# Kernel tuning notes

Measured on AMD Instinct MI355X. Metric: run time of the kernel, lower is better.

Reference implementation:

```python
import jax, jax.numpy as jnp
import numpy as np

BOX = 8.0  # side length of the box points are sampled in
N_POINTS = 12288
N_BINS_TARGET = 10


def setup_inputs() -> dict:
    key = jax.random.key(0)
    k1, k2 = jax.random.split(key)
    pc = jax.random.uniform(k1, (N_POINTS, 3), dtype=jnp.float32) * BOX
    target_rdf = jax.random.uniform(k2, (N_BINS_TARGET,), dtype=jnp.float32) * 2.0
    return {"reconstructed_pc": pc, "target_rdf": target_rdf, "r_max": 10, "dr": 1.0}


def _calculate_rdf(pc, r_max, dr):
    # pc: [N, 3]. r_max, dr are static Python scalars.
    n = pc.shape[0]
    nbins = int(round(float(r_max) / float(dr)))  # len(arange(0, r_max+dr, dr)) - 1
    # Pairwise Euclidean distances via the Gram-matrix trick (same math as torch.cdist p=2).
    sq = jnp.sum(pc * pc, axis=1)                               # [N]
    d2 = sq[:, None] + sq[None, :] - 2.0 * (pc @ pc.T)          # [N, N]
    d = jnp.sqrt(jnp.maximum(d2, 0.0)).ravel()                  # [N*N]
    # torch.histc(bins=nbins, min=0, max=r_max): uniform bins, max value inclusive in last bin.
    idx = jnp.clip(jnp.floor(d / dr).astype(jnp.int32), 0, nbins - 1)
    w = (d <= r_max).astype(jnp.float32)                        # d >= 0 always holds
    hist = jax.ops.segment_sum(w, idx, num_segments=nbins)      # [nbins]
    r_mid = (jnp.arange(nbins, dtype=jnp.float32) + 0.5) * dr
    density = n / (4.0 / 3.0 * jnp.pi * float(r_max) ** 3)
    ideal_counts = 4.0 * jnp.pi * r_mid ** 2 * dr * density * n
    rdf = hist / ideal_counts
    rdf = jnp.where(jnp.isnan(rdf), 0.0, rdf)
    return rdf, r_mid


def reference(reconstructed_pc, target_rdf, r_max, dr):
    rdf, _ = _calculate_rdf(reconstructed_pc, r_max, dr)
    m = min(int(target_rdf.shape[0]), int(rdf.shape[0]))
    diff = rdf[:m] - target_rdf[:m]
    return jnp.mean(diff * diff)
```

## Files before the change

kernel.cpp:

```cpp
#include <hip/hip_runtime.h>


#define BLOCK    256
#define HPAD     17
#define NROWB    16
#define NB       10
#define SLOT     16
#define FP32_SAT 16777216u

__device__ __forceinline__ int row_start(int r, int T) {
    return r * T - ((r * (r - 1)) >> 1);
}

__global__ __launch_bounds__(BLOCK) void rdf_hist_kernel(
    const float* __restrict__ pc, const int* __restrict__ rmaxp,
    const float* __restrict__ drp, unsigned int* __restrict__ part,
    int n, int T)
{
    __shared__ float4 sj[BLOCK];
    __shared__ unsigned int lh[BLOCK * HPAD];
    __shared__ unsigned int sacc[NB];

    const int tid = threadIdx.x;
    const int bid = (int)blockIdx.x;

    const float tf = (float)T;
    float disc = (2.f*tf + 1.f)*(2.f*tf + 1.f) - 8.f*(float)bid;
    int ti = (int)((2.f*tf + 1.f - sqrtf(disc)) * 0.5f);
    ti = max(0, min(ti, T - 1));
    while (ti > 0 && row_start(ti, T) > bid) --ti;
    while (row_start(ti + 1, T) <= bid) ++ti;
    const int tj = ti + (bid - row_start(ti, T));

    const float inv_dr = 1.0f / (*drp);

    #pragma unroll
    for (int k = 0; k < HPAD; ++k) lh[tid * HPAD + k] = 0u;
    if (tid < NB) sacc[tid] = 0u;

    {
        const int j = tj * BLOCK + tid;
        float x = 0.f, y = 0.f, z = 0.f, s = 3.0e30f;
        if (j < n) { x = pc[3*j]; y = pc[3*j+1]; z = pc[3*j+2]; s = x*x + y*y + z*z; }
        sj[tid] = make_float4(x, y, z, s);
    }
    const int i = ti * BLOCK + tid;
    float xi = 0.f, yi = 0.f, zi = 0.f, sqi = 3.0e30f;
    if (i < n) { xi = pc[3*i]; yi = pc[3*i+1]; zi = pc[3*i+2]; sqi = xi*xi + yi*yi + zi*zi; }
    const float m2x = -2.f*xi, m2y = -2.f*yi, m2z = -2.f*zi;

    __syncthreads();

    unsigned int* myrow = &lh[tid * HPAD];

    if (ti == tj) {
        #pragma unroll 8
        for (int j = 0; j < BLOCK; ++j) {
            float4 p = sj[j];
            float d2 = sqi + p.w;
            d2 = fmaf(m2x, p.x, d2);
            d2 = fmaf(m2y, p.y, d2);
            d2 = fmaf(m2z, p.z, d2);
            d2 = (j > tid) ? d2 : 3.0e30f;
            float d = __builtin_amdgcn_sqrtf(d2) * inv_dr;
            unsigned int b = (unsigned int)fminf(d, (float)(NROWB - 1));
            atomicAdd(&myrow[b], 1u);
        }
    } else {
        #pragma unroll 8
        for (int j = 0; j < BLOCK; ++j) {
            float4 p = sj[j];
            float d2 = sqi + p.w;
            d2 = fmaf(m2x, p.x, d2);
            d2 = fmaf(m2y, p.y, d2);
            d2 = fmaf(m2z, p.z, d2);
            float d = __builtin_amdgcn_sqrtf(d2) * inv_dr;
            unsigned int b = (unsigned int)fminf(d, (float)(NROWB - 1));
            atomicAdd(&myrow[b], 1u);
        }
    }

    unsigned int v[NB];
    #pragma unroll
    for (int k = 0; k < NB; ++k) v[k] = myrow[k];
    #pragma unroll
    for (int k = 0; k < NB; ++k) {
        unsigned int s = v[k];
        #pragma unroll
        for (int m = 32; m >= 1; m >>= 1) s += (unsigned int)__shfl_xor((int)s, m, 64);
        v[k] = s;
    }
    if ((tid & 63) == 0) {
        #pragma unroll
        for (int k = 0; k < NB; ++k) atomicAdd(&sacc[k], v[k]);
    }
    __syncthreads();
    if (tid < NB) part[bid * SLOT + tid] = sacc[tid];
}

__global__ __launch_bounds__(BLOCK) void rdf_reduce_loss_kernel(
    const unsigned int* __restrict__ part, const float* __restrict__ target,
    const int* __restrict__ rmaxp, const float* __restrict__ drp,
    float* __restrict__ out, int n, int mt, int nblocks)
{
    __shared__ unsigned int sacc[NB];
    const int tid = threadIdx.x;
    if (tid < NB) sacc[tid] = 0u;
    __syncthreads();

    unsigned int a[NB];
    #pragma unroll
    for (int k = 0; k < NB; ++k) a[k] = 0u;
    for (int i = tid; i < nblocks; i += BLOCK) {
        #pragma unroll
        for (int k = 0; k < NB; ++k) a[k] += part[i * SLOT + k];
    }
    #pragma unroll
    for (int k = 0; k < NB; ++k) {
        unsigned int s = a[k];
        #pragma unroll
        for (int m = 32; m >= 1; m >>= 1) s += (unsigned int)__shfl_xor((int)s, m, 64);
        if ((tid & 63) == 0) atomicAdd(&sacc[k], s);
    }
    __syncthreads();

    if (tid == 0) {
        const float PI = 3.14159265358979323846f;
        const float rmax = (float)(*rmaxp);
        const float dr   = *drp;
        int nbins = (int)roundf(rmax / dr);
        if (nbins > NB) nbins = NB;
        const float density = (float)n / (4.0f / 3.0f * PI * rmax * rmax * rmax);
        const int m = (mt < nbins) ? mt : nbins;
        float acc = 0.0f;
        for (int b = 0; b < m; ++b) {
            unsigned int hb = 2u * sacc[b] + ((b == 0) ? (unsigned int)n : 0u);
            if (hb > FP32_SAT) hb = FP32_SAT;
            float r_mid = ((float)b + 0.5f) * dr;
            float ideal = 4.0f * PI * r_mid * r_mid * dr * density * (float)n;
            float rdf  = (ideal != 0.0f) ? ((float)hb / ideal) : 0.0f;
            float diff = rdf - target[b];
            acc = fmaf(diff, diff, acc);
        }
        out[0] = acc / (float)m;
    }
}

extern "C" void kernel_launch(void* const* d_in, const int* in_sizes, int n_in,
                              void* d_out, int out_size, void* d_ws, size_t ws_size,
                              hipStream_t stream)
{
    const float* pc     = (const float*)d_in[0];
    const float* target = (const float*)d_in[1];
    const int*   rmaxp  = (const int*)d_in[2];
    const float* drp    = (const float*)d_in[3];
    const int n  = in_sizes[0] / 3;
    const int mt = in_sizes[1];

    unsigned int* part = (unsigned int*)d_ws;
    const int T = (n + BLOCK - 1) / BLOCK;
    const int nblocks = T * (T + 1) / 2;

    rdf_hist_kernel<<<nblocks, BLOCK, 0, stream>>>(pc, rmaxp, drp, part, n, T);
    rdf_reduce_loss_kernel<<<1, BLOCK, 0, stream>>>(part, target, rmaxp, drp,
                                                    (float*)d_out, n, mt, nblocks);
}
```

Before: 45.11 us.

## Replace per-thread LDS atomic histogram with packed 6-bit register counters

Each thread now counts bin hits in a 64-bit register holding 6-bit fields per bin, summing 32 pairs before unpacking into register counters. This removes the per-pair shared-memory atomic add and the large padded LDS histogram array. Coordinates are also prescaled by 1/dr so the per-pair multiply disappears, and padding points are placed far apart. The cost is that the packing relies on fewer than 64 hits per bin per 32-pair chunk, and prescaling changes floating-point rounding near bin edges.

```diff
diff --git a/kernel.cpp b/kernel.cpp
--- a/kernel.cpp
+++ b/kernel.cpp
@@ -2,8 +2,6 @@
 
 
 #define BLOCK    256
-#define HPAD     17
-#define NROWB    16
 #define NB       10
 #define SLOT     16
 #define FP32_SAT 16777216u
@@ -12,13 +10,39 @@
     return r * T - ((r * (r - 1)) >> 1);
 }
 
+template <bool DIAG>
+__device__ __forceinline__ void tile_loop(const float4* __restrict__ sj,
+                                          float sqi, float m2x, float m2y, float m2z,
+                                          int tid, unsigned int* c)
+{
+    for (int jc = 0; jc < BLOCK; jc += 32) {
+        unsigned long long cnt = 0ull;
+        #pragma unroll
+        for (int jj = 0; jj < 32; ++jj) {
+            const int j = jc + jj;
+            float4 p = sj[j];
+            float d2 = sqi + p.w;
+            d2 = fmaf(m2x, p.x, d2);
+            d2 = fmaf(m2y, p.y, d2);
+            d2 = fmaf(m2z, p.z, d2);
+            if (DIAG) d2 = (j > tid) ? d2 : 3.0e30f;
+            float d = __builtin_amdgcn_sqrtf(d2);
+            unsigned int b = (unsigned int)d;
+            b = min(b, 10u);
+            cnt += 1ull << (b * 6u);
+        }
+        #pragma unroll
+        for (int k = 0; k < NB; ++k)
+            c[k] += (unsigned int)(cnt >> (6 * k)) & 63u;
+    }
+}
+
 __global__ __launch_bounds__(BLOCK) void rdf_hist_kernel(
     const float* __restrict__ pc, const int* __restrict__ rmaxp,
     const float* __restrict__ drp, unsigned int* __restrict__ part,
     int n, int T)
 {
     __shared__ float4 sj[BLOCK];
-    __shared__ unsigned int lh[BLOCK * HPAD];
     __shared__ unsigned int sacc[NB];
 
     const int tid = threadIdx.x;
@@ -34,65 +58,39 @@
 
     const float inv_dr = 1.0f / (*drp);
 
-    #pragma unroll
-    for (int k = 0; k < HPAD; ++k) lh[tid * HPAD + k] = 0u;
     if (tid < NB) sacc[tid] = 0u;
 
     {
         const int j = tj * BLOCK + tid;
-        float x = 0.f, y = 0.f, z = 0.f, s = 3.0e30f;
-        if (j < n) { x = pc[3*j]; y = pc[3*j+1]; z = pc[3*j+2]; s = x*x + y*y + z*z; }
-        sj[tid] = make_float4(x, y, z, s);
+        float x = -3.0e4f, y = -3.0e4f, z = -3.0e4f;
+        if (j < n) { x = pc[3*j] * inv_dr; y = pc[3*j+1] * inv_dr; z = pc[3*j+2] * inv_dr; }
+        sj[tid] = make_float4(x, y, z, x*x + y*y + z*z);
     }
     const int i = ti * BLOCK + tid;
-    float xi = 0.f, yi = 0.f, zi = 0.f, sqi = 3.0e30f;
-    if (i < n) { xi = pc[3*i]; yi = pc[3*i+1]; zi = pc[3*i+2]; sqi = xi*xi + yi*yi + zi*zi; }
+    float xi = 3.0e4f, yi = 3.0e4f, zi = 3.0e4f;
+    if (i < n) { xi = pc[3*i] * inv_dr; yi = pc[3*i+1] * inv_dr; zi = pc[3*i+2] * inv_dr; }
+    const float sqi = xi*xi + yi*yi + zi*zi;
     const float m2x = -2.f*xi, m2y = -2.f*yi, m2z = -2.f*zi;
 
     __syncthreads();
 
-    unsigned int* myrow = &lh[tid * HPAD];
+    unsigned int c[NB];
+    #pragma unroll
+    for (int k = 0; k < NB; ++k) c[k] = 0u;
 
-    if (ti == tj) {
-        #pragma unroll 8
-        for (int j = 0; j < BLOCK; ++j) {
-            float4 p = sj[j];
-            float d2 = sqi + p.w;
-            d2 = fmaf(m2x, p.x, d2);
-            d2 = fmaf(m2y, p.y, d2);
-            d2 = fmaf(m2z, p.z, d2);
-            d2 = (j > tid) ? d2 : 3.0e30f;
-            float d = __builtin_amdgcn_sqrtf(d2) * inv_dr;
-            unsigned int b = (unsigned int)fminf(d, (float)(NROWB - 1));
-            atomicAdd(&myrow[b], 1u);
-        }
-    } else {
-        #pragma unroll 8
-        for (int j = 0; j < BLOCK; ++j) {
-            float4 p = sj[j];
-            float d2 = sqi + p.w;
-            d2 = fmaf(m2x, p.x, d2);
-            d2 = fmaf(m2y, p.y, d2);
-            d2 = fmaf(m2z, p.z, d2);
-            float d = __builtin_amdgcn_sqrtf(d2) * inv_dr;
-            unsigned int b = (unsigned int)fminf(d, (float)(NROWB - 1));
-            atomicAdd(&myrow[b], 1u);
-        }
-    }
+    if (ti == tj) tile_loop<true >(sj, sqi, m2x, m2y, m2z, tid, c);
+    else          tile_loop<false>(sj, sqi, m2x, m2y, m2z, tid, c);
 
-    unsigned int v[NB];
-    #pragma unroll
-    for (int k = 0; k < NB; ++k) v[k] = myrow[k];
     #pragma unroll
     for (int k = 0; k < NB; ++k) {
-        unsigned int s = v[k];
+        unsigned int s = c[k];
         #pragma unroll
         for (int m = 32; m >= 1; m >>= 1) s += (unsigned int)__shfl_xor((int)s, m, 64);
-        v[k] = s;
+        c[k] = s;
     }
     if ((tid & 63) == 0) {
         #pragma unroll
-        for (int k = 0; k < NB; ++k) atomicAdd(&sacc[k], v[k]);
+        for (int k = 0; k < NB; ++k) atomicAdd(&sacc[k], c[k]);
     }
     __syncthreads();
     if (tid < NB) part[bid * SLOT + tid] = sacc[tid];
```

Result: faster. 40.50 us (-10.2%).
